# Performance work log

Measured on AMD Instinct MI355X. Metric: run time of the kernel, lower is better.

Reference implementation:

```python
import jax, jax.numpy as jnp
import numpy as np

D = 512
SCALE = float(np.sqrt(D // 8))  # sqrt(d_k), d_k = d_model/num_heads = 64
EPS = 1e-5


def _ln(x, g, b):
    m = jnp.mean(x, axis=-1, keepdims=True)
    v = jnp.var(x, axis=-1, keepdims=True)
    return (x - m) * jax.lax.rsqrt(v + EPS) * g + b


def setup_inputs() -> dict:
    key = jax.random.key(0)
    ks = jax.random.split(key, 12)
    B, S = 512, 512
    w = lambda k, shp: jax.random.normal(k, shp, dtype=jnp.float32) * 0.02
    return {
        "sentiment_vec": jax.random.normal(ks[0], (B, D), dtype=jnp.float32),
        "price_sequence": jax.random.normal(ks[1], (B, S, D), dtype=jnp.float32),
        "Wq": w(ks[2], (D, D)), "bq": jnp.zeros((D,), jnp.float32),
        "Wk": w(ks[3], (D, D)), "bk": jnp.zeros((D,), jnp.float32),
        "Wv": w(ks[4], (D, D)), "bv": jnp.zeros((D,), jnp.float32),
        "Wo": w(ks[5], (D, D)), "bo": jnp.zeros((D,), jnp.float32),
        "Wg": w(ks[6], (2 * D, D)), "bg": jnp.zeros((D,), jnp.float32),
        "g_q": jnp.ones((D,), jnp.float32), "beta_q": jnp.zeros((D,), jnp.float32),
        "g_kv": jnp.ones((D,), jnp.float32), "beta_kv": jnp.zeros((D,), jnp.float32),
    }


def reference(sentiment_vec, price_sequence, Wq, bq, Wk, bk, Wv, bv, Wo, bo,
              Wg, bg, g_q, beta_q, g_kv, beta_kv):
    # LayerNorms (query is a single token per batch element)
    Q = _ln(sentiment_vec, g_q, beta_q)            # [B, D]
    KV = _ln(price_sequence, g_kv, beta_kv)        # [B, S, D]
    # Projections (note: forward never splits heads -> single-head attention)
    q = Q @ Wq + bq                                # [B, D]
    k = KV @ Wk + bk                               # [B, S, D]
    v = KV @ Wv + bv                               # [B, S, D]
    # Single-query attention
    scores = jnp.einsum('bd,bsd->bs', q, k) / SCALE
    attn = jax.nn.softmax(scores, axis=-1)         # [B, S] (dropout: eval mode)
    ctx = jnp.einsum('bs,bsd->bd', attn, v)        # [B, D]
    ctx = ctx @ Wo + bo
    # Sigmoid gate over concat([sentiment, context])
    gate_in = jnp.concatenate([sentiment_vec, ctx], axis=-1)  # [B, 2D]
    alpha = jax.nn.sigmoid(gate_in @ Wg + bg)
    fused = alpha * ctx + (1.0 - alpha) * sentiment_vec
    return fused, attn
```

## Files before the change

### kernel.cpp

```cpp
#include <hip/hip_runtime.h>

#define NB 512
#define NS 512
#define ND 512
#define INV_SCALE 0.125f
#define LN_EPS 1e-5f

typedef __attribute__((ext_vector_type(8))) short short8;
typedef __attribute__((ext_vector_type(4))) short short4v;
typedef __attribute__((ext_vector_type(4))) float float4v;

static __device__ __forceinline__ unsigned short f2bf(float x) {
    unsigned int u = __float_as_uint(x);
    unsigned int r = (u + 0x7fffu + ((u >> 16) & 1u)) >> 16;
    return (unsigned short)r;
}
static __device__ __forceinline__ float bf2f(unsigned short h) {
    return __uint_as_float(((unsigned int)h) << 16);
}

__global__ __launch_bounds__(64) void ln_rows_k(const float* __restrict__ x,
                                                const float* __restrict__ g,
                                                const float* __restrict__ be,
                                                float* __restrict__ y) {
    const int row = blockIdx.x;
    const int lane = threadIdx.x;
    const float* xr = x + (size_t)row * ND;
    float4 x0 = *(const float4*)(xr + 4 * lane);
    float4 x1 = *(const float4*)(xr + 256 + 4 * lane);
    float s1 = x0.x + x0.y + x0.z + x0.w + x1.x + x1.y + x1.z + x1.w;
    float s2 = x0.x * x0.x + x0.y * x0.y + x0.z * x0.z + x0.w * x0.w +
               x1.x * x1.x + x1.y * x1.y + x1.z * x1.z + x1.w * x1.w;
    for (int off = 32; off; off >>= 1) {
        s1 += __shfl_xor(s1, off, 64);
        s2 += __shfl_xor(s2, off, 64);
    }
    float mean = s1 * (1.f / 512.f);
    float rstd = rsqrtf(s2 * (1.f / 512.f) - mean * mean + LN_EPS);
    float4 g0 = *(const float4*)(g + 4 * lane);
    float4 g1 = *(const float4*)(g + 256 + 4 * lane);
    float4 b0 = *(const float4*)(be + 4 * lane);
    float4 b1 = *(const float4*)(be + 256 + 4 * lane);
    float4 y0, y1;
    y0.x = (x0.x - mean) * rstd * g0.x + b0.x;
    y0.y = (x0.y - mean) * rstd * g0.y + b0.y;
    y0.z = (x0.z - mean) * rstd * g0.z + b0.z;
    y0.w = (x0.w - mean) * rstd * g0.w + b0.w;
    y1.x = (x1.x - mean) * rstd * g1.x + b1.x;
    y1.y = (x1.y - mean) * rstd * g1.y + b1.y;
    y1.z = (x1.z - mean) * rstd * g1.z + b1.z;
    y1.w = (x1.w - mean) * rstd * g1.w + b1.w;
    float* yr = y + (size_t)row * ND;
    *(float4*)(yr + 4 * lane) = y0;
    *(float4*)(yr + 256 + 4 * lane) = y1;
}

__global__ __launch_bounds__(64) void rowdot_k(const float* __restrict__ q,
                                               const float* __restrict__ bk,
                                               float* __restrict__ s0) {
    const int row = blockIdx.x;
    const int lane = threadIdx.x;
    const float* qr = q + (size_t)row * ND;
    float4 a0 = *(const float4*)(qr + 4 * lane);
    float4 a1 = *(const float4*)(qr + 256 + 4 * lane);
    float4 c0 = *(const float4*)(bk + 4 * lane);
    float4 c1 = *(const float4*)(bk + 256 + 4 * lane);
    float d = a0.x * c0.x + a0.y * c0.y + a0.z * c0.z + a0.w * c0.w +
              a1.x * c1.x + a1.y * c1.y + a1.z * c1.z + a1.w * c1.w;
    for (int off = 32; off; off >>= 1) d += __shfl_xor(d, off, 64);
    if (lane == 0) s0[row] = d;
}

template <bool TRANS_B, int EPI>
__global__ __launch_bounds__(256) void gemm_split_k(
    const float* __restrict__ A1, const float* __restrict__ A2, int ksplit,
    const float* __restrict__ B, const float* __restrict__ bias,
    float* __restrict__ C, int M, int N, int K,
    const float* __restrict__ e_ctx, const float* __restrict__ e_sent) {
    constexpr int LDK = 40;
    __shared__ __align__(16) unsigned short Ah[64 * LDK];
    __shared__ __align__(16) unsigned short Al[64 * LDK];
    __shared__ __align__(16) unsigned short Bh[64 * LDK];
    __shared__ __align__(16) unsigned short Bl[64 * LDK];
    const int t = threadIdx.x;
    const int wave = t >> 6, lane = t & 63;
    const int m0 = blockIdx.y * 64, n0 = blockIdx.x * 64;

    float4v acc[4];
#pragma unroll
    for (int i = 0; i < 4; ++i) acc[i] = (float4v){0.f, 0.f, 0.f, 0.f};

    const int arow = 16 * wave + (lane & 15);
    const int kq8 = (lane >> 4) * 8;

    for (int k0 = 0; k0 < K; k0 += 32) {
#pragma unroll
        for (int h = 0; h < 2; ++h) {
            int f = t + h * 256;
            int row = f >> 3, kq = (f & 7) * 4;
            int kg = k0 + kq;
            float4 v;
            if (kg < ksplit)
                v = *(const float4*)(A1 + (size_t)(m0 + row) * ksplit + kg);
            else
                v = *(const float4*)(A2 + (size_t)(m0 + row) * (K - ksplit) + (kg - ksplit));
            unsigned short h0 = f2bf(v.x), h1 = f2bf(v.y), h2 = f2bf(v.z), h3 = f2bf(v.w);
            short4v hv = {(short)h0, (short)h1, (short)h2, (short)h3};
            short4v lv = {(short)f2bf(v.x - bf2f(h0)), (short)f2bf(v.y - bf2f(h1)),
                          (short)f2bf(v.z - bf2f(h2)), (short)f2bf(v.w - bf2f(h3))};
            *(short4v*)&Ah[row * LDK + kq] = hv;
            *(short4v*)&Al[row * LDK + kq] = lv;
        }
        if (TRANS_B) {
#pragma unroll
            for (int h = 0; h < 2; ++h) {
                int f = t + h * 256;
                int row = f >> 3, kq = (f & 7) * 4;
                float4 v = *(const float4*)(B + (size_t)(n0 + row) * K + k0 + kq);
                unsigned short h0 = f2bf(v.x), h1 = f2bf(v.y), h2 = f2bf(v.z), h3 = f2bf(v.w);
                short4v hv = {(short)h0, (short)h1, (short)h2, (short)h3};
                short4v lv = {(short)f2bf(v.x - bf2f(h0)), (short)f2bf(v.y - bf2f(h1)),
                              (short)f2bf(v.z - bf2f(h2)), (short)f2bf(v.w - bf2f(h3))};
                *(short4v*)&Bh[row * LDK + kq] = hv;
                *(short4v*)&Bl[row * LDK + kq] = lv;
            }
        } else {
#pragma unroll
            for (int h = 0; h < 2; ++h) {
                int f = t + h * 256;
                int krow = f >> 4, nq = (f & 15) * 4;
                float4 v = *(const float4*)(B + (size_t)(k0 + krow) * N + n0 + nq);
                float vv[4] = {v.x, v.y, v.z, v.w};
#pragma unroll
                for (int j = 0; j < 4; ++j) {
                    unsigned short hh = f2bf(vv[j]);
                    Bh[(nq + j) * LDK + krow] = hh;
                    Bl[(nq + j) * LDK + krow] = f2bf(vv[j] - bf2f(hh));
                }
            }
        }
        __syncthreads();
        short8 ah = *(const short8*)&Ah[arow * LDK + kq8];
        short8 al = *(const short8*)&Al[arow * LDK + kq8];
#pragma unroll
        for (int nt = 0; nt < 4; ++nt) {
            int brow = 16 * nt + (lane & 15);
            short8 bh = *(const short8*)&Bh[brow * LDK + kq8];
            short8 bl = *(const short8*)&Bl[brow * LDK + kq8];
            acc[nt] = __builtin_amdgcn_mfma_f32_16x16x32_bf16(ah, bh, acc[nt], 0, 0, 0);
            acc[nt] = __builtin_amdgcn_mfma_f32_16x16x32_bf16(ah, bl, acc[nt], 0, 0, 0);
            acc[nt] = __builtin_amdgcn_mfma_f32_16x16x32_bf16(al, bh, acc[nt], 0, 0, 0);
        }
        __syncthreads();
    }

    const int coln = lane & 15, rbase = (lane >> 4) * 4;
#pragma unroll
    for (int nt = 0; nt < 4; ++nt) {
        int n = n0 + 16 * nt + coln;
        float bv = bias ? bias[n] : 0.f;
#pragma unroll
        for (int r = 0; r < 4; ++r) {
            int m = m0 + 16 * wave + rbase + r;
            float val = acc[nt][r] + bv;
            if (EPI == 1) {
                float a = 1.f / (1.f + __expf(-val));
                float cx = e_ctx[(size_t)m * N + n];
                float sv = e_sent[(size_t)m * N + n];
                val = a * cx + (1.f - a) * sv;
            }
            C[(size_t)m * N + n] = val;
        }
    }
}

__global__ __launch_bounds__(512) void flash_k(const float* __restrict__ ps,
                                               const float* __restrict__ g,
                                               const float* __restrict__ be,
                                               const float* __restrict__ qp,
                                               const float* __restrict__ s0v,
                                               float* __restrict__ ctx_pre,
                                               float* __restrict__ attn) {
    const int b = blockIdx.x;
    const int t = threadIdx.x;
    const int wave = t >> 6, lane = t & 63;
    __shared__ float zbuf[NS];
    __shared__ float ubuf[8][ND];
    __shared__ float lw[8], tw[8];

    const float* qb = qp + (size_t)b * ND;
    float4 q0 = *(const float4*)(qb + 4 * lane);
    float4 q1 = *(const float4*)(qb + 256 + 4 * lane);
    float4 g0 = *(const float4*)(g + 4 * lane);
    float4 g1 = *(const float4*)(g + 256 + 4 * lane);
    float4 b0 = *(const float4*)(be + 4 * lane);
    float4 b1 = *(const float4*)(be + 256 + 4 * lane);

    float4 qg0, qg1;
    qg0.x = g0.x * q0.x; qg0.y = g0.y * q0.y; qg0.z = g0.z * q0.z; qg0.w = g0.w * q0.w;
    qg1.x = g1.x * q1.x; qg1.y = g1.y * q1.y; qg1.z = g1.z * q1.z; qg1.w = g1.w * q1.w;
    float c1 = qg0.x + qg0.y + qg0.z + qg0.w + qg1.x + qg1.y + qg1.z + qg1.w;
    float c2 = b0.x * q0.x + b0.y * q0.y + b0.z * q0.z + b0.w * q0.w +
               b1.x * q1.x + b1.y * q1.y + b1.z * q1.z + b1.w * q1.w;
    for (int off = 32; off; off >>= 1) {
        c1 += __shfl_xor(c1, off, 64);
        c2 += __shfl_xor(c2, off, 64);
    }
    const float K2 = INV_SCALE * (c2 + s0v[b]);
    const float C1 = c1;

    float l = 0.f, t1 = 0.f;
    float4 u0 = {0.f, 0.f, 0.f, 0.f}, u1 = {0.f, 0.f, 0.f, 0.f};

    const float* base = ps + ((size_t)b * NS + wave * 64) * ND + 4 * lane;
    float4 xa0 = *(const float4*)(base);
    float4 xa1 = *(const float4*)(base + 256);
    float4 xb0 = *(const float4*)(base + ND);
    float4 xb1 = *(const float4*)(base + ND + 256);

    for (int r = 0; r < 64; r += 2) {
        float4 ya0, ya1, yb0, yb1;
        if (r < 62) {
            const float* nb = base + (size_t)(r + 2) * ND;
            ya0 = *(const float4*)(nb);
            ya1 = *(const float4*)(nb + 256);
            yb0 = *(const float4*)(nb + ND);
            yb1 = *(const float4*)(nb + ND + 256);
        } else {
            ya0 = xa0; ya1 = xa1; yb0 = xb0; yb1 = xb1;
        }
        float sa1 = xa0.x + xa0.y + xa0.z + xa0.w + xa1.x + xa1.y + xa1.z + xa1.w;
        float sb1 = xb0.x + xb0.y + xb0.z + xb0.w + xb1.x + xb1.y + xb1.z + xb1.w;
        float sa2 = xa0.x * xa0.x + xa0.y * xa0.y + xa0.z * xa0.z + xa0.w * xa0.w +
                    xa1.x * xa1.x + xa1.y * xa1.y + xa1.z * xa1.z + xa1.w * xa1.w;
        float sb2 = xb0.x * xb0.x + xb0.y * xb0.y + xb0.z * xb0.z + xb0.w * xb0.w +
                    xb1.x * xb1.x + xb1.y * xb1.y + xb1.z * xb1.z + xb1.w * xb1.w;
        float sa3 = xa0.x * qg0.x + xa0.y * qg0.y + xa0.z * qg0.z + xa0.w * qg0.w +
                    xa1.x * qg1.x + xa1.y * qg1.y + xa1.z * qg1.z + xa1.w * qg1.w;
        float sb3 = xb0.x * qg0.x + xb0.y * qg0.y + xb0.z * qg0.z + xb0.w * qg0.w +
                    xb1.x * qg1.x + xb1.y * qg1.y + xb1.z * qg1.z + xb1.w * qg1.w;
        for (int off = 32; off; off >>= 1) {
            sa1 += __shfl_xor(sa1, off, 64);
            sb1 += __shfl_xor(sb1, off, 64);
            sa2 += __shfl_xor(sa2, off, 64);
            sb2 += __shfl_xor(sb2, off, 64);
            sa3 += __shfl_xor(sa3, off, 64);
            sb3 += __shfl_xor(sb3, off, 64);
        }
        float meana = sa1 * (1.f / 512.f), meanb = sb1 * (1.f / 512.f);
        float rstda = rsqrtf(sa2 * (1.f / 512.f) - meana * meana + LN_EPS);
        float rstdb = rsqrtf(sb2 * (1.f / 512.f) - meanb * meanb + LN_EPS);
        float za = INV_SCALE * rstda * (sa3 - meana * C1) + K2;
        float zb = INV_SCALE * rstdb * (sb3 - meanb * C1) + K2;
        float pa = __expf(za), pb = __expf(zb);
        l += pa + pb;
        float pra = pa * rstda, prb = pb * rstdb;
        t1 += pra * meana + prb * meanb;
        u0.x += pra * xa0.x + prb * xb0.x;
        u0.y += pra * xa0.y + prb * xb0.y;
        u0.z += pra * xa0.z + prb * xb0.z;
        u0.w += pra * xa0.w + prb * xb0.w;
        u1.x += pra * xa1.x + prb * xb1.x;
        u1.y += pra * xa1.y + prb * xb1.y;
        u1.z += pra * xa1.z + prb * xb1.z;
        u1.w += pra * xa1.w + prb * xb1.w;
        if (lane == 0) {
            zbuf[wave * 64 + r] = za;
            zbuf[wave * 64 + r + 1] = zb;
        }
        xa0 = ya0; xa1 = ya1; xb0 = yb0; xb1 = yb1;
    }

    *(float4*)&ubuf[wave][4 * lane] = u0;
    *(float4*)&ubuf[wave][256 + 4 * lane] = u1;
    if (lane == 0) { lw[wave] = l; tw[wave] = t1; }
    __syncthreads();

    float U = 0.f;
#pragma unroll
    for (int w = 0; w < 8; ++w) U += ubuf[w][t];
    float L = 0.f, T = 0.f;
#pragma unroll
    for (int w = 0; w < 8; ++w) { L += lw[w]; T += tw[w]; }
    float invL = 1.f / L;
    ctx_pre[(size_t)b * ND + t] = g[t] * (U - T) * invL + be[t];
    attn[(size_t)b * NS + t] = __expf(zbuf[t]) * invL;
}

extern "C" void kernel_launch(void* const* d_in, const int* in_sizes, int n_in,
                              void* d_out, int out_size, void* d_ws, size_t ws_size,
                              hipStream_t stream) {
    const float* sent = (const float*)d_in[0];
    const float* ps   = (const float*)d_in[1];
    const float* Wq = (const float*)d_in[2];
    const float* bq = (const float*)d_in[3];
    const float* Wk = (const float*)d_in[4];
    const float* bk = (const float*)d_in[5];
    const float* Wv = (const float*)d_in[6];
    const float* bv = (const float*)d_in[7];
    const float* Wo = (const float*)d_in[8];
    const float* bo = (const float*)d_in[9];
    const float* Wg = (const float*)d_in[10];
    const float* bg = (const float*)d_in[11];
    const float* g_q = (const float*)d_in[12];
    const float* beta_q = (const float*)d_in[13];
    const float* g_kv = (const float*)d_in[14];
    const float* beta_kv = (const float*)d_in[15];

    float* out = (float*)d_out;
    float* attn = out + NB * ND;

    float* ws = (float*)d_ws;
    float* Qln     = ws;
    float* q       = ws + 262144;
    float* qprime  = ws + 524288;
    float* s0      = ws + 786432;
    float* ctx_pre = ws + 786944;
    float* ctx1    = ws + 1049088;
    float* ctx2    = ws + 1311232;

    dim3 ggrid(8, 8);

    ln_rows_k<<<NB, 64, 0, stream>>>(sent, g_q, beta_q, Qln);
    gemm_split_k<false, 0><<<ggrid, 256, 0, stream>>>(
        Qln, nullptr, 512, Wq, bq, q, 512, 512, 512, nullptr, nullptr);
    rowdot_k<<<NB, 64, 0, stream>>>(q, bk, s0);
    gemm_split_k<true, 0><<<ggrid, 256, 0, stream>>>(
        q, nullptr, 512, Wk, nullptr, qprime, 512, 512, 512, nullptr, nullptr);

    flash_k<<<NB, 512, 0, stream>>>(ps, g_kv, beta_kv, qprime, s0, ctx_pre, attn);

    gemm_split_k<false, 0><<<ggrid, 256, 0, stream>>>(
        ctx_pre, nullptr, 512, Wv, bv, ctx1, 512, 512, 512, nullptr, nullptr);
    gemm_split_k<false, 0><<<ggrid, 256, 0, stream>>>(
        ctx1, nullptr, 512, Wo, bo, ctx2, 512, 512, 512, nullptr, nullptr);

    gemm_split_k<false, 1><<<ggrid, 256, 0, stream>>>(
        sent, ctx2, 512, Wg, bg, out, 512, 512, 1024, ctx2, sent);
}
```

Measured before the change: 848.8 us.

## Shrink GEMM tiles to 32x32 and prefetch next K-slice into registers

The small 512x512 GEMMs switch from 64x64 tiles (64 blocks) to 32x32 tiles (256 blocks), with each wave owning one 16x16 sub-tile, so more CUs have work. The global loads for the next K-slice are also issued before the MFMA phase, so their latency overlaps with compute. In exchange each block reuses less data and issues more global loads per flop.

```diff
diff --git a/kernel.cpp b/kernel.cpp
--- a/kernel.cpp
+++ b/kernel.cpp
@@ -72,105 +72,107 @@
 }
 
 template <bool TRANS_B, int EPI>
-__global__ __launch_bounds__(256) void gemm_split_k(
+__global__ __launch_bounds__(256) void gemm32_k(
     const float* __restrict__ A1, const float* __restrict__ A2, int ksplit,
     const float* __restrict__ B, const float* __restrict__ bias,
     float* __restrict__ C, int M, int N, int K,
     const float* __restrict__ e_ctx, const float* __restrict__ e_sent) {
     constexpr int LDK = 40;
-    __shared__ __align__(16) unsigned short Ah[64 * LDK];
-    __shared__ __align__(16) unsigned short Al[64 * LDK];
-    __shared__ __align__(16) unsigned short Bh[64 * LDK];
-    __shared__ __align__(16) unsigned short Bl[64 * LDK];
+    __shared__ __align__(16) unsigned short Ah[32 * LDK];
+    __shared__ __align__(16) unsigned short Al[32 * LDK];
+    __shared__ __align__(16) unsigned short Bh[32 * LDK];
+    __shared__ __align__(16) unsigned short Bl[32 * LDK];
     const int t = threadIdx.x;
     const int wave = t >> 6, lane = t & 63;
-    const int m0 = blockIdx.y * 64, n0 = blockIdx.x * 64;
-
-    float4v acc[4];
+    const int m0 = blockIdx.y * 32, n0 = blockIdx.x * 32;
+    const int wm = (wave & 1) * 16, wn = (wave >> 1) * 16;
+
+    float4v acc = (float4v){0.f, 0.f, 0.f, 0.f};
+
+    const int arow = wm + (lane & 15);
+    const int brow = wn + (lane & 15);
+    const int kq8 = (lane >> 4) * 8;
+
+    const int srow = t >> 3, skq = (t & 7) * 4;
+
+    float4 va, vb;
+    {
+        int kg = skq;
+        if (kg < ksplit)
+            va = *(const float4*)(A1 + (size_t)(m0 + srow) * ksplit + kg);
+        else
+            va = *(const float4*)(A2 + (size_t)(m0 + srow) * (K - ksplit) + (kg - ksplit));
+        if (TRANS_B)
+            vb = *(const float4*)(B + (size_t)(n0 + srow) * K + skq);
+        else
+            vb = *(const float4*)(B + (size_t)srow * N + n0 + skq);
+    }
+
+    for (int k0 = 0; k0 < K; k0 += 32) {
+        {
+            unsigned short h0 = f2bf(va.x), h1 = f2bf(va.y), h2 = f2bf(va.z), h3 = f2bf(va.w);
+            short4v hv = {(short)h0, (short)h1, (short)h2, (short)h3};
+            short4v lv = {(short)f2bf(va.x - bf2f(h0)), (short)f2bf(va.y - bf2f(h1)),
+                          (short)f2bf(va.z - bf2f(h2)), (short)f2bf(va.w - bf2f(h3))};
+            *(short4v*)&Ah[srow * LDK + skq] = hv;
+            *(short4v*)&Al[srow * LDK + skq] = lv;
+        }
+        if (TRANS_B) {
+            unsigned short h0 = f2bf(vb.x), h1 = f2bf(vb.y), h2 = f2bf(vb.z), h3 = f2bf(vb.w);
+            short4v hv = {(short)h0, (short)h1, (short)h2, (short)h3};
+            short4v lv = {(short)f2bf(vb.x - bf2f(h0)), (short)f2bf(vb.y - bf2f(h1)),
+                          (short)f2bf(vb.z - bf2f(h2)), (short)f2bf(vb.w - bf2f(h3))};
+            *(short4v*)&Bh[srow * LDK + skq] = hv;
+            *(short4v*)&Bl[srow * LDK + skq] = lv;
+        } else {
+            float vv[4] = {vb.x, vb.y, vb.z, vb.w};
 #pragma unroll
-    for (int i = 0; i < 4; ++i) acc[i] = (float4v){0.f, 0.f, 0.f, 0.f};
-
-    const int arow = 16 * wave + (lane & 15);
-    const int kq8 = (lane >> 4) * 8;
-
-    for (int k0 = 0; k0 < K; k0 += 32) {
-#pragma unroll
-        for (int h = 0; h < 2; ++h) {
-            int f = t + h * 256;
-            int row = f >> 3, kq = (f & 7) * 4;
-            int kg = k0 + kq;
-            float4 v;
+            for (int j = 0; j < 4; ++j) {
+                unsigned short hh = f2bf(vv[j]);
+                Bh[(skq + j) * LDK + srow] = hh;
+                Bl[(skq + j) * LDK + srow] = f2bf(vv[j] - bf2f(hh));
+            }
+        }
+        float4 va2, vb2;
+        if (k0 + 32 < K) {
+            int kg = k0 + 32 + skq;
             if (kg < ksplit)
-                v = *(const float4*)(A1 + (size_t)(m0 + row) * ksplit + kg);
+                va2 = *(const float4*)(A1 + (size_t)(m0 + srow) * ksplit + kg);
             else
-                v = *(const float4*)(A2 + (size_t)(m0 + row) * (K - ksplit) + (kg - ksplit));
-            unsigned short h0 = f2bf(v.x), h1 = f2bf(v.y), h2 = f2bf(v.z), h3 = f2bf(v.w);
-            short4v hv = {(short)h0, (short)h1, (short)h2, (short)h3};
-            short4v lv = {(short)f2bf(v.x - bf2f(h0)), (short)f2bf(v.y - bf2f(h1)),
-                          (short)f2bf(v.z - bf2f(h2)), (short)f2bf(v.w - bf2f(h3))};
-            *(short4v*)&Ah[row * LDK + kq] = hv;
-            *(short4v*)&Al[row * LDK + kq] = lv;
-        }
-        if (TRANS_B) {
-#pragma unroll
-            for (int h = 0; h < 2; ++h) {
-                int f = t + h * 256;
-                int row = f >> 3, kq = (f & 7) * 4;
-                float4 v = *(const float4*)(B + (size_t)(n0 + row) * K + k0 + kq);
-                unsigned short h0 = f2bf(v.x), h1 = f2bf(v.y), h2 = f2bf(v.z), h3 = f2bf(v.w);
-                short4v hv = {(short)h0, (short)h1, (short)h2, (short)h3};
-                short4v lv = {(short)f2bf(v.x - bf2f(h0)), (short)f2bf(v.y - bf2f(h1)),
-                              (short)f2bf(v.z - bf2f(h2)), (short)f2bf(v.w - bf2f(h3))};
-                *(short4v*)&Bh[row * LDK + kq] = hv;
-                *(short4v*)&Bl[row * LDK + kq] = lv;
-            }
+                va2 = *(const float4*)(A2 + (size_t)(m0 + srow) * (K - ksplit) + (kg - ksplit));
+            if (TRANS_B)
+                vb2 = *(const float4*)(B + (size_t)(n0 + srow) * K + k0 + 32 + skq);
+            else
+                vb2 = *(const float4*)(B + (size_t)(k0 + 32 + srow) * N + n0 + skq);
         } else {
-#pragma unroll
-            for (int h = 0; h < 2; ++h) {
-                int f = t + h * 256;
-                int krow = f >> 4, nq = (f & 15) * 4;
-                float4 v = *(const float4*)(B + (size_t)(k0 + krow) * N + n0 + nq);
-                float vv[4] = {v.x, v.y, v.z, v.w};
-#pragma unroll
-                for (int j = 0; j < 4; ++j) {
-                    unsigned short hh = f2bf(vv[j]);
-                    Bh[(nq + j) * LDK + krow] = hh;
-                    Bl[(nq + j) * LDK + krow] = f2bf(vv[j] - bf2f(hh));
-                }
-            }
+            va2 = va; vb2 = vb;
         }
         __syncthreads();
         short8 ah = *(const short8*)&Ah[arow * LDK + kq8];
         short8 al = *(const short8*)&Al[arow * LDK + kq8];
+        short8 bh = *(const short8*)&Bh[brow * LDK + kq8];
+        short8 bl = *(const short8*)&Bl[brow * LDK + kq8];
+        acc = __builtin_amdgcn_mfma_f32_16x16x32_bf16(ah, bh, acc, 0, 0, 0);
+        acc = __builtin_amdgcn_mfma_f32_16x16x32_bf16(ah, bl, acc, 0, 0, 0);
+        acc = __builtin_amdgcn_mfma_f32_16x16x32_bf16(al, bh, acc, 0, 0, 0);
+        __syncthreads();
+        va = va2; vb = vb2;
+    }
+
+    const int coln = lane & 15, rbase = (lane >> 4) * 4;
+    const int n = n0 + wn + coln;
+    const float bv = bias ? bias[n] : 0.f;
 #pragma unroll
-        for (int nt = 0; nt < 4; ++nt) {
-            int brow = 16 * nt + (lane & 15);
-            short8 bh = *(const short8*)&Bh[brow * LDK + kq8];
-            short8 bl = *(const short8*)&Bl[brow * LDK + kq8];
-            acc[nt] = __builtin_amdgcn_mfma_f32_16x16x32_bf16(ah, bh, acc[nt], 0, 0, 0);
-            acc[nt] = __builtin_amdgcn_mfma_f32_16x16x32_bf16(ah, bl, acc[nt], 0, 0, 0);
-            acc[nt] = __builtin_amdgcn_mfma_f32_16x16x32_bf16(al, bh, acc[nt], 0, 0, 0);
-        }
-        __syncthreads();
-    }
-
-    const int coln = lane & 15, rbase = (lane >> 4) * 4;
-#pragma unroll
-    for (int nt = 0; nt < 4; ++nt) {
-        int n = n0 + 16 * nt + coln;
-        float bv = bias ? bias[n] : 0.f;
-#pragma unroll
-        for (int r = 0; r < 4; ++r) {
-            int m = m0 + 16 * wave + rbase + r;
-            float val = acc[nt][r] + bv;
-            if (EPI == 1) {
-                float a = 1.f / (1.f + __expf(-val));
-                float cx = e_ctx[(size_t)m * N + n];
-                float sv = e_sent[(size_t)m * N + n];
-                val = a * cx + (1.f - a) * sv;
-            }
-            C[(size_t)m * N + n] = val;
-        }
+    for (int r = 0; r < 4; ++r) {
+        int m = m0 + wm + rbase + r;
+        float val = acc[r] + bv;
+        if (EPI == 1) {
+            float a = 1.f / (1.f + __expf(-val));
+            float cx = e_ctx[(size_t)m * N + n];
+            float sv = e_sent[(size_t)m * N + n];
+            val = a * cx + (1.f - a) * sv;
+        }
+        C[(size_t)m * N + n] = val;
     }
 }
 
@@ -319,22 +321,22 @@
     float* ctx1    = ws + 1049088;
     float* ctx2    = ws + 1311232;
 
-    dim3 ggrid(8, 8);
+    dim3 g32(16, 16);
 
     ln_rows_k<<<NB, 64, 0, stream>>>(sent, g_q, beta_q, Qln);
-    gemm_split_k<false, 0><<<ggrid, 256, 0, stream>>>(
+    gemm32_k<false, 0><<<g32, 256, 0, stream>>>(
         Qln, nullptr, 512, Wq, bq, q, 512, 512, 512, nullptr, nullptr);
     rowdot_k<<<NB, 64, 0, stream>>>(q, bk, s0);
-    gemm_split_k<true, 0><<<ggrid, 256, 0, stream>>>(
+    gemm32_k<true, 0><<<g32, 256, 0, stream>>>(
         q, nullptr, 512, Wk, nullptr, qprime, 512, 512, 512, nullptr, nullptr);
 
     flash_k<<<NB, 512, 0, stream>>>(ps, g_kv, beta_kv, qprime, s0, ctx_pre, attn);
 
-    gemm_split_k<false, 0><<<ggrid, 256, 0, stream>>>(
+    gemm32_k<false, 0><<<g32, 256, 0, stream>>>(
         ctx_pre, nullptr, 512, Wv, bv, ctx1, 512, 512, 512, nullptr, nullptr);
-    gemm_split_k<false, 0><<<ggrid, 256, 0, stream>>>(
+    gemm32_k<false, 0><<<g32, 256, 0, stream>>>(
         ctx1, nullptr, 512, Wo, bo, ctx2, 512, 512, 512, nullptr, nullptr);
 
-    gemm_split_k<false, 1><<<ggrid, 256, 0, stream>>>(
+    gemm32_k<false, 1><<<g32, 256, 0, stream>>>(
         sent, ctx2, 512, Wg, bg, out, 512, 512, 1024, ctx2, sent);
 }
```

Result: faster. 791.7 us (-6.7%).
